# Performance work log

Hardware: AMD Instinct MI355X
Metric: run time of the kernel (lower is better)

Reference implementation:

```python
import jax, jax.numpy as jnp
import numpy as np

STRIDE = 1
PAD = 1
K = 3
BN_EPS = 1e-5


def conv2d(x, w, b, stride, padding):
    out = jax.lax.conv_general_dilated(
        x, w, (stride, stride), [(padding, padding), (padding, padding)],
        dimension_numbers=("NCHW", "OIHW", "NCHW"))
    return out + b[None, :, None, None]


def _bilinear_gather(xb, sy, sx):
    # Zero-fill outside bounds (torchvision DeformConv2d semantics).
    Hin, Win = xb.shape[1], xb.shape[2]
    y0 = jnp.floor(sy)
    x0 = jnp.floor(sx)
    y1 = y0 + 1.0
    x1 = x0 + 1.0
    wy1 = sy - y0
    wy0 = 1.0 - wy1
    wx1 = sx - x0
    wx0 = 1.0 - wx1

    def g(yi, xi):
        valid = (yi >= 0) & (yi < Hin) & (xi >= 0) & (xi < Win)
        yc = jnp.clip(yi, 0, Hin - 1).astype(jnp.int32)
        xc = jnp.clip(xi, 0, Win - 1).astype(jnp.int32)
        v = xb[:, yc, xc]  # [C, K2, Hout, Wout]
        return v * valid[None].astype(xb.dtype)

    return (g(y0, x0) * (wy0 * wx0)[None] + g(y0, x1) * (wy0 * wx1)[None]
            + g(y1, x0) * (wy1 * wx0)[None] + g(y1, x1) * (wy1 * wx1)[None])


def deform_conv2d(x, offset, w, b, stride, padding):
    B, C, Hin, Win = x.shape
    O = w.shape[0]
    K2 = K * K
    Hout, Wout = offset.shape[2], offset.shape[3]
    # torchvision layout: channel 2*k = dy, 2*k+1 = dx, k row-major over kernel
    off = offset.reshape(B, K2, 2, Hout, Wout)
    dy, dx = off[:, :, 0], off[:, :, 1]
    ki, kj = jnp.meshgrid(jnp.arange(K), jnp.arange(K), indexing="ij")
    ki = ki.reshape(K2).astype(x.dtype)
    kj = kj.reshape(K2).astype(x.dtype)
    oy = (jnp.arange(Hout) * stride - padding).astype(x.dtype)
    ox = (jnp.arange(Wout) * stride - padding).astype(x.dtype)
    sy = ki[None, :, None, None] + oy[None, None, :, None] + dy  # [B,K2,Hout,Wout]
    sx = kj[None, :, None, None] + ox[None, None, None, :] + dx
    sampled = jax.vmap(_bilinear_gather)(x, sy, sx)  # [B, C, K2, Hout, Wout]
    out = jnp.einsum("bckhw,ock->bohw", sampled, w.reshape(O, C, K2))
    return out + b[None, :, None, None]


def batchnorm_train(x, gamma, beta):
    # training-mode BN: biased batch stats over (N, H, W)
    mean = jnp.mean(x, axis=(0, 2, 3), keepdims=True)
    var = jnp.mean(jnp.square(x - mean), axis=(0, 2, 3), keepdims=True)
    xn = (x - mean) * jax.lax.rsqrt(var + BN_EPS)
    return xn * gamma[None, :, None, None] + beta[None, :, None, None]


def setup_inputs() -> dict:
    key = jax.random.key(0)
    ks = jax.random.split(key, 4)
    B, C, H, W = 8, 64, 128, 128
    O = 64
    x = jax.random.normal(ks[0], (B, C, H, W), dtype=jnp.float32)
    fan_off = C * K * K
    offset_w = jax.random.normal(ks[1], (2 * K * K, C, K, K), dtype=jnp.float32) / np.sqrt(fan_off)
    offset_b = jnp.zeros((2 * K * K,), dtype=jnp.float32)
    deform_w = jax.random.normal(ks[2], (O, C, K, K), dtype=jnp.float32) / np.sqrt(fan_off)
    deform_b = jnp.zeros((O,), dtype=jnp.float32)
    bn_gamma = jnp.ones((O,), dtype=jnp.float32)
    bn_beta = jnp.zeros((O,), dtype=jnp.float32)
    prelu_a = jnp.full((1,), 0.2, dtype=jnp.float32)
    return {"x": x, "offset_w": offset_w, "offset_b": offset_b,
            "deform_w": deform_w, "deform_b": deform_b,
            "bn_gamma": bn_gamma, "bn_beta": bn_beta, "prelu_a": prelu_a}


def reference(x, offset_w, offset_b, deform_w, deform_b, bn_gamma, bn_beta, prelu_a):
    offset = conv2d(x, offset_w, offset_b, STRIDE, PAD)
    y = deform_conv2d(x, offset, deform_w, deform_b, STRIDE, PAD)
    y = batchnorm_train(y, bn_gamma, bn_beta)
    return jnp.where(y >= 0, y, prelu_a[0] * y)
```

## Files before the change

### kernel.cpp

```cpp
#include <hip/hip_runtime.h>
#include <hip/hip_bf16.h>
#include <hip/hip_fp16.h>

typedef float f32x4 __attribute__((ext_vector_type(4)));
typedef unsigned int u32;
typedef u32 u32x4 __attribute__((ext_vector_type(4)));
typedef __bf16 bf16x8 __attribute__((ext_vector_type(8)));
typedef short s16x8 __attribute__((ext_vector_type(8)));
typedef unsigned short u16;

#define HWSZ 16384
#define NPIX 131072

#define XT_OFF    0u
#define PART_OFF  33554432u
#define WB_OFF    42991616u
#define STATS_OFF 43106816u
#define WO_OFF    43107840u

__device__ inline u32 pkbf(float lo, float hi) {
  u16 l = __builtin_bit_cast(u16, __float2bfloat16(lo));
  u16 h = __builtin_bit_cast(u16, __float2bfloat16(hi));
  return (u32)l | ((u32)h << 16);
}
__device__ inline float bflo(u32 u) { return __builtin_bit_cast(float, u << 16); }
__device__ inline float bfhi(u32 u) { return __builtin_bit_cast(float, u & 0xFFFF0000u); }

__global__ void kprep(const float* __restrict__ dw, const float* __restrict__ ow,
                      u16* __restrict__ Wb, u16* __restrict__ Wo) {
  int t = blockIdx.x * 256 + threadIdx.x;
  if (t < 36864) {
    int o = t / 576, r = t % 576;
    int c = r / 9, k2 = r % 9;
    __hip_bfloat16 h = __float2bfloat16(dw[t]);
    Wb[o * 576 + k2 * 64 + c] = __builtin_bit_cast(u16, h);
  } else if (t < 55296) {
    int t2 = t - 36864;
    int oc = t2 / 576, r = t2 % 576;
    int c = r / 9, k2 = r % 9;
    float v = (oc < 18) ? ow[(oc * 64 + c) * 9 + k2] : 0.f;
    __hip_bfloat16 h = __float2bfloat16(v);
    Wo[oc * 576 + k2 * 64 + c] = __builtin_bit_cast(u16, h);
  }
}

__global__ void ktrans(const float* __restrict__ x, u16* __restrict__ xt) {
  __shared__ float tile[64][65];
  int blk = blockIdx.x;
  int b = blk >> 8, hwT = (blk & 255) * 64;
  int tid = threadIdx.x;
  int tx = tid & 63, ty = tid >> 6;
  const float* xp = x + (size_t)b * 64 * HWSZ;
#pragma unroll
  for (int r = 0; r < 16; ++r) {
    int c = r * 4 + ty;
    tile[c][tx] = xp[c * HWSZ + hwT + tx];
  }
  __syncthreads();
  u16* xo = xt + ((size_t)b * HWSZ + hwT) * 64;
  int o8 = (tid & 7) * 8;
#pragma unroll
  for (int r = 0; r < 2; ++r) {
    int hwl = r * 32 + (tid >> 3);
    u32x4 out;
#pragma unroll
    for (int j = 0; j < 4; ++j)
      out[j] = pkbf(tile[o8 + 2 * j][hwl], tile[o8 + 2 * j + 1][hwl]);
    *(u32x4*)&xo[(size_t)hwl * 64 + o8] = out;
  }
}

__global__ __launch_bounds__(256, 6) void kmain(
    const u16* __restrict__ xt, const u16* __restrict__ Wo,
    const float* __restrict__ offb, const u16* __restrict__ Wb,
    const float* __restrict__ db, float* __restrict__ y,
    float* __restrict__ part) {
  __shared__ u16 S2[2][64 * 64];
  __shared__ float OFFT[64 * 20];
  __shared__ u32 mWp[576 * 2];
  __shared__ u32 mPos[576];
  int tid = threadIdx.x;
  int lane = tid & 63, wid = tid >> 6;
  int bid = blockIdx.x;
  int batch = bid & 7, tilei = bid >> 3;
  int base = (batch << 14) + tilei * 64;
  int b = batch;
  int hw0 = base & 16383;
  int h0 = hw0 >> 7, w0 = hw0 & 127;

  int oct = lane & 7;
  int p0 = wid * 8 + (lane >> 3);
  int oct16 = oct << 4, oct8 = oct << 3;
  int q8 = (lane >> 4) * 8;
  const char* xb = (const char*)xt;

  int ocb2 = wid & 1, pxb2 = (wid >> 1) * 2;
  int orow_o = ocb2 * 16 + (lane & 15);
  f32x4 acco0 = {0.f, 0.f, 0.f, 0.f}, acco1 = {0.f, 0.f, 0.f, 0.f};
#pragma unroll
  for (int k = 0; k < 9; ++k) {
#pragma unroll
    for (int pi = 0; pi < 2; ++pi) {
      int pp = p0 + pi * 32;
      int yy = h0 - 1 + k / 3, xx = w0 + pp - 1 + k % 3;
      bool v = ((unsigned)yy < 128u) && ((unsigned)xx < 128u);
      const char* pb =
          v ? xb + (size_t)(((b << 14) + yy * 128 + xx) * 128) + oct16 : xb;
      u32x4 g = *(const u32x4*)pb;
      u32 msk = v ? 0xFFFFFFFFu : 0u;
      u32x4 out;
#pragma unroll
      for (int j = 0; j < 4; ++j) out[j] = g[j] & msk;
      *(u32x4*)&S2[k & 1][(pp * 64 + oct8) ^ ((pp & 7) << 3)] = out;
    }
    __syncthreads();
#pragma unroll
    for (int h = 0; h < 2; ++h) {
      int kc = 2 * k + h;
      s16x8 a = *(const s16x8*)(Wo + orow_o * 576 + kc * 32 + q8);
      {
        int row = pxb2 * 16 + (lane & 15);
        int idx = (row * 64 + h * 32 + q8) ^ ((row & 7) << 3);
        bf16x8 bb = __builtin_bit_cast(bf16x8, *(const s16x8*)&S2[k & 1][idx]);
        acco0 = __builtin_amdgcn_mfma_f32_16x16x32_bf16(
            __builtin_bit_cast(bf16x8, a), bb, acco0, 0, 0, 0);
      }
      {
        int row = (pxb2 + 1) * 16 + (lane & 15);
        int idx = (row * 64 + h * 32 + q8) ^ ((row & 7) << 3);
        bf16x8 bb = __builtin_bit_cast(bf16x8, *(const s16x8*)&S2[k & 1][idx]);
        acco1 = __builtin_amdgcn_mfma_f32_16x16x32_bf16(
            __builtin_bit_cast(bf16x8, a), bb, acco1, 0, 0, 0);
      }
    }
  }
  __syncthreads();

#pragma unroll
  for (int t2 = 0; t2 < 2; ++t2) {
    int pixl = (pxb2 + t2) * 16 + (lane & 15);
    int ocb = ocb2 * 16 + (lane >> 4) * 4;
    f32x4 a = t2 ? acco1 : acco0;
#pragma unroll
    for (int r = 0; r < 4; ++r) {
      int oc = ocb + r;
      if (oc < 18) OFFT[pixl * 20 + oc] = a[r] + offb[oc];
    }
  }
  __syncthreads();

  for (int t = tid; t < 576; t += 256) {
    int tp = t / 9, k2 = t - tp * 9;
    int pix = base + tp;
    int hw = pix & 16383;
    int hh = hw >> 7, ww = hw & 127;
    float dy = OFFT[tp * 20 + 2 * k2];
    float dx = OFFT[tp * 20 + 2 * k2 + 1];
    float sy = (float)(hh - 1 + k2 / 3) + dy;
    float sx = (float)(ww - 1 + k2 % 3) + dx;
    float fy = floorf(sy), fx = floorf(sx);
    int y0 = (int)fy, x0 = (int)fx;
    float wy1 = sy - fy, wx1 = sx - fx;
    float ay0 = ((unsigned)y0 < 128u) ? 1.f - wy1 : 0.f;
    float ay1 = ((unsigned)(y0 + 1) < 128u) ? wy1 : 0.f;
    float ax0 = ((unsigned)x0 < 128u) ? 1.f - wx1 : 0.f;
    float ax1 = ((unsigned)(x0 + 1) < 128u) ? wx1 : 0.f;
    int y0c = min(max(y0, 0), 127), x0c = min(max(x0, 0), 127);
    int dys = min(max(y0 + 1, 0), 127) - y0c;
    int dxs = min(max(x0 + 1, 0), 127) - x0c;
    mWp[t * 2]     = __builtin_bit_cast(u32, __floats2half2_rn(ay0 * ax0, ay0 * ax1));
    mWp[t * 2 + 1] = __builtin_bit_cast(u32, __floats2half2_rn(ay1 * ax0, ay1 * ax1));
    mPos[t] = (u32)(((b << 14) + y0c * 128 + x0c) * 128) | (u32)dxs | ((u32)dys << 1);
  }
  __syncthreads();

  f32x4 acc[4];
#pragma unroll
  for (int nb = 0; nb < 4; ++nb) acc[nb] = {0.f, 0.f, 0.f, 0.f};
  int orow_d = wid * 16 + (lane & 15);
#pragma unroll
  for (int k = 0; k < 9; ++k) {
#pragma unroll
    for (int pi = 0; pi < 2; ++pi) {
      int pp = p0 + pi * 32;
      int t = pp * 9 + k;
      u32 wlo = mWp[t * 2], whi = mWp[t * 2 + 1];
      u32 pm = mPos[t];
      u32 dxB = (pm & 1u) << 7;
      u32 dyB = (pm & 2u) << 13;
      const char* pb = xb + (pm & 0xFFFFFF80u) + oct16;
      u32x4 c00 = *(const u32x4*)pb;
      u32x4 c01 = *(const u32x4*)(pb + dxB);
      u32x4 c10 = *(const u32x4*)(pb + dyB);
      u32x4 c11 = *(const u32x4*)(pb + dyB + dxB);
      __half2 hl = __builtin_bit_cast(__half2, wlo);
      __half2 hh2 = __builtin_bit_cast(__half2, whi);
      float w00 = __low2float(hl), w01 = __high2float(hl);
      float w10 = __low2float(hh2), w11 = __high2float(hh2);
      u32x4 out;
#pragma unroll
      for (int j = 0; j < 4; ++j) {
        float sL = fmaf(w11, bflo(c11[j]), fmaf(w10, bflo(c10[j]),
                   fmaf(w01, bflo(c01[j]), w00 * bflo(c00[j]))));
        float sH = fmaf(w11, bfhi(c11[j]), fmaf(w10, bfhi(c10[j]),
                   fmaf(w01, bfhi(c01[j]), w00 * bfhi(c00[j]))));
        out[j] = pkbf(sL, sH);
      }
      *(u32x4*)&S2[k & 1][(pp * 64 + oct8) ^ ((pp & 7) << 3)] = out;
    }
    __syncthreads();
#pragma unroll
    for (int h = 0; h < 2; ++h) {
      int kc = 2 * k + h;
      s16x8 a = *(const s16x8*)(Wb + orow_d * 576 + kc * 32 + q8);
#pragma unroll
      for (int nb = 0; nb < 4; ++nb) {
        int row = nb * 16 + (lane & 15);
        int idx = (row * 64 + h * 32 + q8) ^ ((row & 7) << 3);
        bf16x8 bb = __builtin_bit_cast(bf16x8, *(const s16x8*)&S2[k & 1][idx]);
        acc[nb] = __builtin_amdgcn_mfma_f32_16x16x32_bf16(
            __builtin_bit_cast(bf16x8, a), bb, acc[nb], 0, 0, 0);
      }
    }
  }

  int obase = wid * 16 + (lane >> 4) * 4;
  float s1[4] = {0, 0, 0, 0}, s2[4] = {0, 0, 0, 0};
#pragma unroll
  for (int nb = 0; nb < 4; ++nb) {
    int pix = base + nb * 16 + (lane & 15);
    int hw = pix & 16383;
    float* yp = y + (size_t)b * (64 * HWSZ) + hw;
#pragma unroll
    for (int r = 0; r < 4; ++r) {
      int o = obase + r;
      float v = acc[nb][r] + db[o];
      yp[(size_t)o * HWSZ] = v;
      s1[r] += v;
      s2[r] += v * v;
    }
  }
#pragma unroll
  for (int m = 1; m < 16; m <<= 1) {
#pragma unroll
    for (int r = 0; r < 4; ++r) {
      s1[r] += __shfl_xor(s1[r], m, 64);
      s2[r] += __shfl_xor(s2[r], m, 64);
    }
  }
  if ((lane & 15) == 0) {
    float* pp = part + (size_t)bid * 128;
#pragma unroll
    for (int r = 0; r < 4; ++r) {
      pp[obase + r] = s1[r];
      pp[64 + obase + r] = s2[r];
    }
  }
}

__global__ void kbnf(const float* __restrict__ part, const float* __restrict__ gamma,
                     const float* __restrict__ beta, float* __restrict__ stats) {
  __shared__ float r1[256], r2[256];
  int o = blockIdx.x;
  int tid = threadIdx.x;
  float s1 = 0.f, s2 = 0.f;
  for (int i = tid; i < 2048; i += 256) {
    s1 += part[(size_t)i * 128 + o];
    s2 += part[(size_t)i * 128 + 64 + o];
  }
  r1[tid] = s1; r2[tid] = s2;
  __syncthreads();
  for (int s = 128; s > 0; s >>= 1) {
    if (tid < s) { r1[tid] += r1[tid + s]; r2[tid] += r2[tid + s]; }
    __syncthreads();
  }
  if (tid == 0) {
    float m = r1[0] * (1.f / 131072.f);
    float v = r2[0] * (1.f / 131072.f) - m * m;
    float sc = gamma[o] * rsqrtf(v + 1e-5f);
    stats[128 + o] = sc;
    stats[192 + o] = beta[o] - m * sc;
  }
}

__global__ void kfinal(float* __restrict__ y, const float* __restrict__ stats,
                       const float* __restrict__ pa) {
  float a = pa[0];
  int total = NPIX * 64 / 4;
  for (int i = blockIdx.x * blockDim.x + threadIdx.x; i < total;
       i += gridDim.x * blockDim.x) {
    int o = (i >> 12) & 63;
    f32x4 v = ((const f32x4*)y)[i];
    float sc = stats[128 + o], sh = stats[192 + o];
#pragma unroll
    for (int j = 0; j < 4; ++j) {
      float t = fmaf(v[j], sc, sh);
      v[j] = t >= 0.f ? t : a * t;
    }
    ((f32x4*)y)[i] = v;
  }
}

extern "C" void kernel_launch(void* const* d_in, const int* in_sizes, int n_in,
                              void* d_out, int out_size, void* d_ws, size_t ws_size,
                              hipStream_t stream) {
  const float* x  = (const float*)d_in[0];
  const float* ow = (const float*)d_in[1];
  const float* ob = (const float*)d_in[2];
  const float* dw = (const float*)d_in[3];
  const float* db = (const float*)d_in[4];
  const float* gm = (const float*)d_in[5];
  const float* bt = (const float*)d_in[6];
  const float* pa = (const float*)d_in[7];
  char* ws = (char*)d_ws;
  u16*   xt    = (u16*)(ws + XT_OFF);
  float* part  = (float*)(ws + PART_OFF);
  u16*   Wb    = (u16*)(ws + WB_OFF);
  u16*   Wo    = (u16*)(ws + WO_OFF);
  float* stats = (float*)(ws + STATS_OFF);
  float* y = (float*)d_out;

  kprep<<<216, 256, 0, stream>>>(dw, ow, Wb, Wo);
  ktrans<<<2048, 256, 0, stream>>>(x, xt);
  kmain<<<2048, 256, 0, stream>>>(xt, Wo, ob, Wb, db, y, part);
  kbnf<<<64, 256, 0, stream>>>(part, gm, bt, stats);
  kfinal<<<2048, 256, 0, stream>>>(y, stats, pa);
}
```

Baseline: 98.11 us.

## Prefetch next tap's global gathers into registers and relax occupancy bound

Both the offset-conv im2col loop and the deformable bilinear-gather loop are software-pipelined. The global loads for tap k+1 are issued into a second register set before tap k is blended and stored to shared memory, so memory latency overlaps the MFMA work. To make room for the extra live registers, the launch-bounds occupancy hint drops from 6 to 4 blocks. The OFFT offset table is aliased onto the S2 staging buffer to cut shared memory. The risk is that fewer resident waves hide latency worse than the explicit prefetch recovers it.

Measured after the change: 97.92 us. No clear change (-0.2%).

```diff
diff --git a/kernel.cpp b/kernel.cpp
--- a/kernel.cpp
+++ b/kernel.cpp
@@ -70,15 +70,15 @@
   }
 }
 
-__global__ __launch_bounds__(256, 6) void kmain(
+__global__ __launch_bounds__(256, 4) void kmain(
     const u16* __restrict__ xt, const u16* __restrict__ Wo,
     const float* __restrict__ offb, const u16* __restrict__ Wb,
     const float* __restrict__ db, float* __restrict__ y,
     float* __restrict__ part) {
   __shared__ u16 S2[2][64 * 64];
-  __shared__ float OFFT[64 * 20];
   __shared__ u32 mWp[576 * 2];
   __shared__ u32 mPos[576];
+  float* OFFT = (float*)&S2[0][0];
   int tid = threadIdx.x;
   int lane = tid & 63, wid = tid >> 6;
   int bid = blockIdx.x;
@@ -97,8 +97,8 @@
   int ocb2 = wid & 1, pxb2 = (wid >> 1) * 2;
   int orow_o = ocb2 * 16 + (lane & 15);
   f32x4 acco0 = {0.f, 0.f, 0.f, 0.f}, acco1 = {0.f, 0.f, 0.f, 0.f};
-#pragma unroll
-  for (int k = 0; k < 9; ++k) {
+
+  auto im_load = [&](int k, u32x4 (&g)[2], u32 (&m)[2]) {
 #pragma unroll
     for (int pi = 0; pi < 2; ++pi) {
       int pp = p0 + pi * 32;
@@ -106,31 +106,53 @@
       bool v = ((unsigned)yy < 128u) && ((unsigned)xx < 128u);
       const char* pb =
           v ? xb + (size_t)(((b << 14) + yy * 128 + xx) * 128) + oct16 : xb;
-      u32x4 g = *(const u32x4*)pb;
-      u32 msk = v ? 0xFFFFFFFFu : 0u;
+      g[pi] = *(const u32x4*)pb;
+      m[pi] = v ? 0xFFFFFFFFu : 0u;
+    }
+  };
+  auto im_store = [&](int k, const u32x4 (&g)[2], const u32 (&m)[2]) {
+#pragma unroll
+    for (int pi = 0; pi < 2; ++pi) {
+      int pp = p0 + pi * 32;
       u32x4 out;
 #pragma unroll
-      for (int j = 0; j < 4; ++j) out[j] = g[j] & msk;
+      for (int j = 0; j < 4; ++j) out[j] = g[pi][j] & m[pi];
       *(u32x4*)&S2[k & 1][(pp * 64 + oct8) ^ ((pp & 7) << 3)] = out;
     }
-    __syncthreads();
-#pragma unroll
-    for (int h = 0; h < 2; ++h) {
-      int kc = 2 * k + h;
-      s16x8 a = *(const s16x8*)(Wo + orow_o * 576 + kc * 32 + q8);
-      {
-        int row = pxb2 * 16 + (lane & 15);
-        int idx = (row * 64 + h * 32 + q8) ^ ((row & 7) << 3);
-        bf16x8 bb = __builtin_bit_cast(bf16x8, *(const s16x8*)&S2[k & 1][idx]);
-        acco0 = __builtin_amdgcn_mfma_f32_16x16x32_bf16(
-            __builtin_bit_cast(bf16x8, a), bb, acco0, 0, 0, 0);
-      }
-      {
-        int row = (pxb2 + 1) * 16 + (lane & 15);
-        int idx = (row * 64 + h * 32 + q8) ^ ((row & 7) << 3);
-        bf16x8 bb = __builtin_bit_cast(bf16x8, *(const s16x8*)&S2[k & 1][idx]);
-        acco1 = __builtin_amdgcn_mfma_f32_16x16x32_bf16(
-            __builtin_bit_cast(bf16x8, a), bb, acco1, 0, 0, 0);
+  };
+
+  {
+    u32x4 gA[2], gB[2];
+    u32 mA[2], mB[2];
+    im_load(0, gA, mA);
+#pragma unroll
+    for (int k = 0; k < 9; ++k) {
+      if (k & 1) {
+        if (k < 8) im_load(k + 1, gA, mA);
+        im_store(k, gB, mB);
+      } else {
+        if (k < 8) im_load(k + 1, gB, mB);
+        im_store(k, gA, mA);
+      }
+      __syncthreads();
+#pragma unroll
+      for (int h = 0; h < 2; ++h) {
+        int kc = 2 * k + h;
+        s16x8 a = *(const s16x8*)(Wo + orow_o * 576 + kc * 32 + q8);
+        {
+          int row = pxb2 * 16 + (lane & 15);
+          int idx = (row * 64 + h * 32 + q8) ^ ((row & 7) << 3);
+          bf16x8 bb = __builtin_bit_cast(bf16x8, *(const s16x8*)&S2[k & 1][idx]);
+          acco0 = __builtin_amdgcn_mfma_f32_16x16x32_bf16(
+              __builtin_bit_cast(bf16x8, a), bb, acco0, 0, 0, 0);
+        }
+        {
+          int row = (pxb2 + 1) * 16 + (lane & 15);
+          int idx = (row * 64 + h * 32 + q8) ^ ((row & 7) << 3);
+          bf16x8 bb = __builtin_bit_cast(bf16x8, *(const s16x8*)&S2[k & 1][idx]);
+          acco1 = __builtin_amdgcn_mfma_f32_16x16x32_bf16(
+              __builtin_bit_cast(bf16x8, a), bb, acco1, 0, 0, 0);
+        }
       }
     }
   }
@@ -178,48 +200,72 @@
 #pragma unroll
   for (int nb = 0; nb < 4; ++nb) acc[nb] = {0.f, 0.f, 0.f, 0.f};
   int orow_d = wid * 16 + (lane & 15);
-#pragma unroll
-  for (int k = 0; k < 9; ++k) {
+
+  auto tap_load = [&](int k, u32x4 (&c)[2][4], u32 (&wl)[2], u32 (&wh)[2]) {
 #pragma unroll
     for (int pi = 0; pi < 2; ++pi) {
       int pp = p0 + pi * 32;
       int t = pp * 9 + k;
-      u32 wlo = mWp[t * 2], whi = mWp[t * 2 + 1];
+      wl[pi] = mWp[t * 2];
+      wh[pi] = mWp[t * 2 + 1];
       u32 pm = mPos[t];
       u32 dxB = (pm & 1u) << 7;
       u32 dyB = (pm & 2u) << 13;
       const char* pb = xb + (pm & 0xFFFFFF80u) + oct16;
-      u32x4 c00 = *(const u32x4*)pb;
-      u32x4 c01 = *(const u32x4*)(pb + dxB);
-      u32x4 c10 = *(const u32x4*)(pb + dyB);
-      u32x4 c11 = *(const u32x4*)(pb + dyB + dxB);
-      __half2 hl = __builtin_bit_cast(__half2, wlo);
-      __half2 hh2 = __builtin_bit_cast(__half2, whi);
+      c[pi][0] = *(const u32x4*)pb;
+      c[pi][1] = *(const u32x4*)(pb + dxB);
+      c[pi][2] = *(const u32x4*)(pb + dyB);
+      c[pi][3] = *(const u32x4*)(pb + dyB + dxB);
+    }
+  };
+  auto tap_store = [&](int k, const u32x4 (&c)[2][4], const u32 (&wl)[2],
+                       const u32 (&wh)[2]) {
+#pragma unroll
+    for (int pi = 0; pi < 2; ++pi) {
+      int pp = p0 + pi * 32;
+      __half2 hl = __builtin_bit_cast(__half2, wl[pi]);
+      __half2 hh2 = __builtin_bit_cast(__half2, wh[pi]);
       float w00 = __low2float(hl), w01 = __high2float(hl);
       float w10 = __low2float(hh2), w11 = __high2float(hh2);
       u32x4 out;
 #pragma unroll
       for (int j = 0; j < 4; ++j) {
-        float sL = fmaf(w11, bflo(c11[j]), fmaf(w10, bflo(c10[j]),
-                   fmaf(w01, bflo(c01[j]), w00 * bflo(c00[j]))));
-        float sH = fmaf(w11, bfhi(c11[j]), fmaf(w10, bfhi(c10[j]),
-                   fmaf(w01, bfhi(c01[j]), w00 * bfhi(c00[j]))));
+        float sL = fmaf(w11, bflo(c[pi][3][j]), fmaf(w10, bflo(c[pi][2][j]),
+                   fmaf(w01, bflo(c[pi][1][j]), w00 * bflo(c[pi][0][j]))));
+        float sH = fmaf(w11, bfhi(c[pi][3][j]), fmaf(w10, bfhi(c[pi][2][j]),
+                   fmaf(w01, bfhi(c[pi][1][j]), w00 * bfhi(c[pi][0][j]))));
         out[j] = pkbf(sL, sH);
       }
       *(u32x4*)&S2[k & 1][(pp * 64 + oct8) ^ ((pp & 7) << 3)] = out;
     }
-    __syncthreads();
-#pragma unroll
-    for (int h = 0; h < 2; ++h) {
-      int kc = 2 * k + h;
-      s16x8 a = *(const s16x8*)(Wb + orow_d * 576 + kc * 32 + q8);
-#pragma unroll
-      for (int nb = 0; nb < 4; ++nb) {
-        int row = nb * 16 + (lane & 15);
-        int idx = (row * 64 + h * 32 + q8) ^ ((row & 7) << 3);
-        bf16x8 bb = __builtin_bit_cast(bf16x8, *(const s16x8*)&S2[k & 1][idx]);
-        acc[nb] = __builtin_amdgcn_mfma_f32_16x16x32_bf16(
-            __builtin_bit_cast(bf16x8, a), bb, acc[nb], 0, 0, 0);
+  };
+
+  {
+    u32x4 cA[2][4], cB[2][4];
+    u32 wlA[2], whA[2], wlB[2], whB[2];
+    tap_load(0, cA, wlA, whA);
+#pragma unroll
+    for (int k = 0; k < 9; ++k) {
+      if (k & 1) {
+        if (k < 8) tap_load(k + 1, cA, wlA, whA);
+        tap_store(k, cB, wlB, whB);
+      } else {
+        if (k < 8) tap_load(k + 1, cB, wlB, whB);
+        tap_store(k, cA, wlA, whA);
+      }
+      __syncthreads();
+#pragma unroll
+      for (int h = 0; h < 2; ++h) {
+        int kc = 2 * k + h;
+        s16x8 a = *(const s16x8*)(Wb + orow_d * 576 + kc * 32 + q8);
+#pragma unroll
+        for (int nb = 0; nb < 4; ++nb) {
+          int row = nb * 16 + (lane & 15);
+          int idx = (row * 64 + h * 32 + q8) ^ ((row & 7) << 3);
+          bf16x8 bb = __builtin_bit_cast(bf16x8, *(const s16x8*)&S2[k & 1][idx]);
+          acc[nb] = __builtin_amdgcn_mfma_f32_16x16x32_bf16(
+              __builtin_bit_cast(bf16x8, a), bb, acc[nb], 0, 0, 0);
+        }
       }
     }
   }
```

## Give each wave its own 16-pixel slice to remove block-wide barriers

Applied to the files above, without the earlier changes.

Reworks the fused offset-conv and deformable-conv kernel so each wave gathers, interpolates and multiplies its own 16 pixels against all output channels, using a per-wave LDS slice. This drops every __syncthreads in the main loops, since each wave only reads LDS data it wrote itself. In exchange, each wave now loads all weight rows from global memory, the launch-bounds occupancy hint drops from 6 to 4, and the BN partial-stats buffer grows fourfold (per wave instead of per block), so the finalize kernel reads more partials.

After: 172.5 us. 1.76x slower.

```diff
diff --git a/kernel.cpp b/kernel.cpp
--- a/kernel.cpp
+++ b/kernel.cpp
@@ -70,12 +70,12 @@
   }
 }
 
-__global__ __launch_bounds__(256, 6) void kmain(
+__global__ __launch_bounds__(256, 4) void kmain(
     const u16* __restrict__ xt, const u16* __restrict__ Wo,
     const float* __restrict__ offb, const u16* __restrict__ Wb,
     const float* __restrict__ db, float* __restrict__ y,
     float* __restrict__ part) {
-  __shared__ u16 S2[2][64 * 64];
+  __shared__ u16 S2[2][4 * 1024];
   __shared__ float OFFT[64 * 20];
   __shared__ u32 mWp[576 * 2];
   __shared__ u32 mPos[576];
@@ -88,74 +88,69 @@
   int hw0 = base & 16383;
   int h0 = hw0 >> 7, w0 = hw0 & 127;
 
-  int oct = lane & 7;
-  int p0 = wid * 8 + (lane >> 3);
-  int oct16 = oct << 4, oct8 = oct << 3;
+  int pl = lane >> 2;
+  int quad = lane & 3;
+  int qb = quad << 5;
+  int q16 = quad << 4;
+  int sw = (pl & 7) << 3;
+  int pxg = w0 + wid * 16 + pl;
   int q8 = (lane >> 4) * 8;
   const char* xb = (const char*)xt;
 
-  int ocb2 = wid & 1, pxb2 = (wid >> 1) * 2;
-  int orow_o = ocb2 * 16 + (lane & 15);
-  f32x4 acco0 = {0.f, 0.f, 0.f, 0.f}, acco1 = {0.f, 0.f, 0.f, 0.f};
+  f32x4 acco[2];
+  acco[0] = {0.f, 0.f, 0.f, 0.f};
+  acco[1] = {0.f, 0.f, 0.f, 0.f};
 #pragma unroll
   for (int k = 0; k < 9; ++k) {
-#pragma unroll
-    for (int pi = 0; pi < 2; ++pi) {
-      int pp = p0 + pi * 32;
-      int yy = h0 - 1 + k / 3, xx = w0 + pp - 1 + k % 3;
+    u16* Sw = &S2[k & 1][wid * 1024];
+    {
+      int yy = h0 - 1 + k / 3, xx = pxg - 1 + k % 3;
       bool v = ((unsigned)yy < 128u) && ((unsigned)xx < 128u);
       const char* pb =
-          v ? xb + (size_t)(((b << 14) + yy * 128 + xx) * 128) + oct16 : xb;
-      u32x4 g = *(const u32x4*)pb;
+          v ? xb + (size_t)(((b << 14) + yy * 128 + xx) * 128) + qb : xb;
+      u32x4 g0 = *(const u32x4*)pb;
+      u32x4 g1 = *(const u32x4*)(pb + 16);
       u32 msk = v ? 0xFFFFFFFFu : 0u;
-      u32x4 out;
-#pragma unroll
-      for (int j = 0; j < 4; ++j) out[j] = g[j] & msk;
-      *(u32x4*)&S2[k & 1][(pp * 64 + oct8) ^ ((pp & 7) << 3)] = out;
-    }
-    __syncthreads();
+      u32x4 o0, o1;
+#pragma unroll
+      for (int j = 0; j < 4; ++j) { o0[j] = g0[j] & msk; o1[j] = g1[j] & msk; }
+      *(u32x4*)&Sw[(pl * 64 + q16) ^ sw] = o0;
+      *(u32x4*)&Sw[(pl * 64 + q16 + 8) ^ sw] = o1;
+    }
 #pragma unroll
     for (int h = 0; h < 2; ++h) {
       int kc = 2 * k + h;
-      s16x8 a = *(const s16x8*)(Wo + orow_o * 576 + kc * 32 + q8);
-      {
-        int row = pxb2 * 16 + (lane & 15);
-        int idx = (row * 64 + h * 32 + q8) ^ ((row & 7) << 3);
-        bf16x8 bb = __builtin_bit_cast(bf16x8, *(const s16x8*)&S2[k & 1][idx]);
-        acco0 = __builtin_amdgcn_mfma_f32_16x16x32_bf16(
-            __builtin_bit_cast(bf16x8, a), bb, acco0, 0, 0, 0);
-      }
-      {
-        int row = (pxb2 + 1) * 16 + (lane & 15);
-        int idx = (row * 64 + h * 32 + q8) ^ ((row & 7) << 3);
-        bf16x8 bb = __builtin_bit_cast(bf16x8, *(const s16x8*)&S2[k & 1][idx]);
-        acco1 = __builtin_amdgcn_mfma_f32_16x16x32_bf16(
-            __builtin_bit_cast(bf16x8, a), bb, acco1, 0, 0, 0);
-      }
-    }
-  }
-  __syncthreads();
-
-#pragma unroll
-  for (int t2 = 0; t2 < 2; ++t2) {
-    int pixl = (pxb2 + t2) * 16 + (lane & 15);
-    int ocb = ocb2 * 16 + (lane >> 4) * 4;
-    f32x4 a = t2 ? acco1 : acco0;
+#pragma unroll
+      for (int ob = 0; ob < 2; ++ob) {
+        s16x8 a = *(const s16x8*)(Wo + (ob * 16 + (lane & 15)) * 576 + kc * 32 + q8);
+        int row = lane & 15;
+        bf16x8 bb = __builtin_bit_cast(
+            bf16x8, *(const s16x8*)&Sw[(row * 64 + h * 32 + q8) ^ ((row & 7) << 3)]);
+        acco[ob] = __builtin_amdgcn_mfma_f32_16x16x32_bf16(
+            __builtin_bit_cast(bf16x8, a), bb, acco[ob], 0, 0, 0);
+      }
+    }
+  }
+
+#pragma unroll
+  for (int ob = 0; ob < 2; ++ob) {
+    int pixl = wid * 16 + (lane & 15);
+    int ocb = ob * 16 + (lane >> 4) * 4;
 #pragma unroll
     for (int r = 0; r < 4; ++r) {
       int oc = ocb + r;
-      if (oc < 18) OFFT[pixl * 20 + oc] = a[r] + offb[oc];
-    }
-  }
-  __syncthreads();
-
-  for (int t = tid; t < 576; t += 256) {
+      if (oc < 18) OFFT[pixl * 20 + oc] = acco[ob][r] + offb[oc];
+    }
+  }
+
+  for (int t = lane; t < 144; t += 64) {
     int tp = t / 9, k2 = t - tp * 9;
-    int pix = base + tp;
+    int pixl = wid * 16 + tp;
+    int pix = base + pixl;
     int hw = pix & 16383;
     int hh = hw >> 7, ww = hw & 127;
-    float dy = OFFT[tp * 20 + 2 * k2];
-    float dx = OFFT[tp * 20 + 2 * k2 + 1];
+    float dy = OFFT[pixl * 20 + 2 * k2];
+    float dx = OFFT[pixl * 20 + 2 * k2 + 1];
     float sy = (float)(hh - 1 + k2 / 3) + dy;
     float sx = (float)(ww - 1 + k2 % 3) + dx;
     float fy = floorf(sy), fx = floorf(sx);
@@ -168,92 +163,105 @@
     int y0c = min(max(y0, 0), 127), x0c = min(max(x0, 0), 127);
     int dys = min(max(y0 + 1, 0), 127) - y0c;
     int dxs = min(max(x0 + 1, 0), 127) - x0c;
-    mWp[t * 2]     = __builtin_bit_cast(u32, __floats2half2_rn(ay0 * ax0, ay0 * ax1));
-    mWp[t * 2 + 1] = __builtin_bit_cast(u32, __floats2half2_rn(ay1 * ax0, ay1 * ax1));
-    mPos[t] = (u32)(((b << 14) + y0c * 128 + x0c) * 128) | (u32)dxs | ((u32)dys << 1);
-  }
-  __syncthreads();
+    int tg = pixl * 9 + k2;
+    mWp[tg * 2]     = __builtin_bit_cast(u32, __floats2half2_rn(ay0 * ax0, ay0 * ax1));
+    mWp[tg * 2 + 1] = __builtin_bit_cast(u32, __floats2half2_rn(ay1 * ax0, ay1 * ax1));
+    mPos[tg] = (u32)(((b << 14) + y0c * 128 + x0c) * 128) | (u32)dxs | ((u32)dys << 1);
+  }
 
   f32x4 acc[4];
 #pragma unroll
-  for (int nb = 0; nb < 4; ++nb) acc[nb] = {0.f, 0.f, 0.f, 0.f};
-  int orow_d = wid * 16 + (lane & 15);
+  for (int ob = 0; ob < 4; ++ob) acc[ob] = {0.f, 0.f, 0.f, 0.f};
 #pragma unroll
   for (int k = 0; k < 9; ++k) {
-#pragma unroll
-    for (int pi = 0; pi < 2; ++pi) {
-      int pp = p0 + pi * 32;
-      int t = pp * 9 + k;
-      u32 wlo = mWp[t * 2], whi = mWp[t * 2 + 1];
-      u32 pm = mPos[t];
+    u16* Sw = &S2[k & 1][wid * 1024];
+    {
+      int tg = (wid * 16 + pl) * 9 + k;
+      u32 wlo = mWp[tg * 2], whi = mWp[tg * 2 + 1];
+      u32 pm = mPos[tg];
       u32 dxB = (pm & 1u) << 7;
       u32 dyB = (pm & 2u) << 13;
-      const char* pb = xb + (pm & 0xFFFFFF80u) + oct16;
-      u32x4 c00 = *(const u32x4*)pb;
-      u32x4 c01 = *(const u32x4*)(pb + dxB);
-      u32x4 c10 = *(const u32x4*)(pb + dyB);
-      u32x4 c11 = *(const u32x4*)(pb + dyB + dxB);
+      const char* pb = xb + (pm & 0xFFFFFF80u) + qb;
+      u32x4 a00 = *(const u32x4*)pb;
+      u32x4 b00 = *(const u32x4*)(pb + 16);
+      u32x4 a01 = *(const u32x4*)(pb + dxB);
+      u32x4 b01 = *(const u32x4*)(pb + dxB + 16);
+      u32x4 a10 = *(const u32x4*)(pb + dyB);
+      u32x4 b10 = *(const u32x4*)(pb + dyB + 16);
+      u32x4 a11 = *(const u32x4*)(pb + dyB + dxB);
+      u32x4 b11 = *(const u32x4*)(pb + dyB + dxB + 16);
       __half2 hl = __builtin_bit_cast(__half2, wlo);
       __half2 hh2 = __builtin_bit_cast(__half2, whi);
       float w00 = __low2float(hl), w01 = __high2float(hl);
       float w10 = __low2float(hh2), w11 = __high2float(hh2);
-      u32x4 out;
+      u32x4 o0, o1;
 #pragma unroll
       for (int j = 0; j < 4; ++j) {
-        float sL = fmaf(w11, bflo(c11[j]), fmaf(w10, bflo(c10[j]),
-                   fmaf(w01, bflo(c01[j]), w00 * bflo(c00[j]))));
-        float sH = fmaf(w11, bfhi(c11[j]), fmaf(w10, bfhi(c10[j]),
-                   fmaf(w01, bfhi(c01[j]), w00 * bfhi(c00[j]))));
-        out[j] = pkbf(sL, sH);
-      }
-      *(u32x4*)&S2[k & 1][(pp * 64 + oct8) ^ ((pp & 7) << 3)] = out;
-    }
-    __syncthreads();
+        float sL = fmaf(w11, bflo(a11[j]), fmaf(w10, bflo(a10[j]),
+                   fmaf(w01, bflo(a01[j]), w00 * bflo(a00[j]))));
+        float sH = fmaf(w11, bfhi(a11[j]), fmaf(w10, bfhi(a10[j]),
+                   fmaf(w01, bfhi(a01[j]), w00 * bfhi(a00[j]))));
+        o0[j] = pkbf(sL, sH);
+        float tL = fmaf(w11, bflo(b11[j]), fmaf(w10, bflo(b10[j]),
+                   fmaf(w01, bflo(b01[j]), w00 * bflo(b00[j]))));
+        float tH = fmaf(w11, bfhi(b11[j]), fmaf(w10, bfhi(b10[j]),
+                   fmaf(w01, bfhi(b01[j]), w00 * bfhi(b00[j]))));
+        o1[j] = pkbf(tL, tH);
+      }
+      *(u32x4*)&Sw[(pl * 64 + q16) ^ sw] = o0;
+      *(u32x4*)&Sw[(pl * 64 + q16 + 8) ^ sw] = o1;
+    }
 #pragma unroll
     for (int h = 0; h < 2; ++h) {
       int kc = 2 * k + h;
-      s16x8 a = *(const s16x8*)(Wb + orow_d * 576 + kc * 32 + q8);
-#pragma unroll
-      for (int nb = 0; nb < 4; ++nb) {
-        int row = nb * 16 + (lane & 15);
-        int idx = (row * 64 + h * 32 + q8) ^ ((row & 7) << 3);
-        bf16x8 bb = __builtin_bit_cast(bf16x8, *(const s16x8*)&S2[k & 1][idx]);
-        acc[nb] = __builtin_amdgcn_mfma_f32_16x16x32_bf16(
-            __builtin_bit_cast(bf16x8, a), bb, acc[nb], 0, 0, 0);
-      }
-    }
-  }
-
-  int obase = wid * 16 + (lane >> 4) * 4;
-  float s1[4] = {0, 0, 0, 0}, s2[4] = {0, 0, 0, 0};
-#pragma unroll
-  for (int nb = 0; nb < 4; ++nb) {
-    int pix = base + nb * 16 + (lane & 15);
-    int hw = pix & 16383;
-    float* yp = y + (size_t)b * (64 * HWSZ) + hw;
+#pragma unroll
+      for (int ob = 0; ob < 4; ++ob) {
+        s16x8 a = *(const s16x8*)(Wb + (ob * 16 + (lane & 15)) * 576 + kc * 32 + q8);
+        int row = lane & 15;
+        bf16x8 bb = __builtin_bit_cast(
+            bf16x8, *(const s16x8*)&Sw[(row * 64 + h * 32 + q8) ^ ((row & 7) << 3)]);
+        acc[ob] = __builtin_amdgcn_mfma_f32_16x16x32_bf16(
+            __builtin_bit_cast(bf16x8, a), bb, acc[ob], 0, 0, 0);
+      }
+    }
+  }
+
+  int pix = base + wid * 16 + (lane & 15);
+  int hw = pix & 16383;
+  float* yp = y + (size_t)b * (64 * HWSZ) + hw;
+  float s1[4][4], s2[4][4];
+#pragma unroll
+  for (int ob = 0; ob < 4; ++ob) {
+    int ocb = ob * 16 + (lane >> 4) * 4;
 #pragma unroll
     for (int r = 0; r < 4; ++r) {
-      int o = obase + r;
-      float v = acc[nb][r] + db[o];
+      int o = ocb + r;
+      float v = acc[ob][r] + db[o];
       yp[(size_t)o * HWSZ] = v;
-      s1[r] += v;
-      s2[r] += v * v;
+      s1[ob][r] = v;
+      s2[ob][r] = v * v;
     }
   }
 #pragma unroll
   for (int m = 1; m < 16; m <<= 1) {
 #pragma unroll
-    for (int r = 0; r < 4; ++r) {
-      s1[r] += __shfl_xor(s1[r], m, 64);
-      s2[r] += __shfl_xor(s2[r], m, 64);
-    }
+    for (int ob = 0; ob < 4; ++ob)
+#pragma unroll
+      for (int r = 0; r < 4; ++r) {
+        s1[ob][r] += __shfl_xor(s1[ob][r], m, 64);
+        s2[ob][r] += __shfl_xor(s2[ob][r], m, 64);
+      }
   }
   if ((lane & 15) == 0) {
-    float* pp = part + (size_t)bid * 128;
-#pragma unroll
-    for (int r = 0; r < 4; ++r) {
-      pp[obase + r] = s1[r];
-      pp[64 + obase + r] = s2[r];
+    float* pp = part + (size_t)bid * 512 + wid * 128;
+#pragma unroll
+    for (int ob = 0; ob < 4; ++ob) {
+      int ocb = ob * 16 + (lane >> 4) * 4;
+#pragma unroll
+      for (int r = 0; r < 4; ++r) {
+        pp[ocb + r] = s1[ob][r];
+        pp[64 + ocb + r] = s2[ob][r];
+      }
     }
   }
 }
@@ -264,7 +272,7 @@
   int o = blockIdx.x;
   int tid = threadIdx.x;
   float s1 = 0.f, s2 = 0.f;
-  for (int i = tid; i < 2048; i += 256) {
+  for (int i = tid; i < 8192; i += 256) {
     s1 += part[(size_t)i * 128 + o];
     s2 += part[(size_t)i * 128 + 64 + o];
   }
```

## Use full-row 128-pixel tiles and stage pre-BN output in bf16

Applied to the files above, without the earlier changes.

Each kmain block now processes a whole 128-pixel image row instead of 64 pixels, which halves the grid and doubles the MFMA work per block, letting one A-fragment load feed more MFMAs. OFFT now aliases the S2 buffer to save shared memory, and occupancy is lowered to 4 blocks. The pre-BN activations are written to a bf16 workspace instead of fp32 output, and the final BN+PReLU pass reads bf16 and expands to fp32, cutting intermediate memory traffic. The cost is extra rounding of pre-normalization values and higher register and LDS pressure per block.

Result: faster. 92.27 us, median of 2 (-5.9%).

```diff
diff --git a/kernel.cpp b/kernel.cpp
--- a/kernel.cpp
+++ b/kernel.cpp
@@ -13,6 +13,7 @@
 #define NPIX 131072
 
 #define XT_OFF    0u
+#define YB_OFF    16777216u
 #define PART_OFF  33554432u
 #define WB_OFF    42991616u
 #define STATS_OFF 43106816u
@@ -70,23 +71,22 @@
   }
 }
 
-__global__ __launch_bounds__(256, 6) void kmain(
+__global__ __launch_bounds__(256, 4) void kmain(
     const u16* __restrict__ xt, const u16* __restrict__ Wo,
     const float* __restrict__ offb, const u16* __restrict__ Wb,
-    const float* __restrict__ db, float* __restrict__ y,
+    const float* __restrict__ db, u16* __restrict__ yb,
     float* __restrict__ part) {
-  __shared__ u16 S2[2][64 * 64];
-  __shared__ float OFFT[64 * 20];
-  __shared__ u32 mWp[576 * 2];
-  __shared__ u32 mPos[576];
+  __shared__ u16 S2[2][128 * 64];
+  __shared__ u32 mWp[1152 * 2];
+  __shared__ u32 mPos[1152];
+  float* OFFT = (float*)&S2[0][0];
   int tid = threadIdx.x;
   int lane = tid & 63, wid = tid >> 6;
   int bid = blockIdx.x;
   int batch = bid & 7, tilei = bid >> 3;
-  int base = (batch << 14) + tilei * 64;
+  int base = (batch << 14) + tilei * 128;
   int b = batch;
-  int hw0 = base & 16383;
-  int h0 = hw0 >> 7, w0 = hw0 & 127;
+  int h0 = tilei;
 
   int oct = lane & 7;
   int p0 = wid * 8 + (lane >> 3);
@@ -94,15 +94,17 @@
   int q8 = (lane >> 4) * 8;
   const char* xb = (const char*)xt;
 
-  int ocb2 = wid & 1, pxb2 = (wid >> 1) * 2;
+  int ocb2 = wid & 1, pxb4 = (wid >> 1) * 4;
   int orow_o = ocb2 * 16 + (lane & 15);
-  f32x4 acco0 = {0.f, 0.f, 0.f, 0.f}, acco1 = {0.f, 0.f, 0.f, 0.f};
+  f32x4 acco[4];
+#pragma unroll
+  for (int t2 = 0; t2 < 4; ++t2) acco[t2] = {0.f, 0.f, 0.f, 0.f};
 #pragma unroll
   for (int k = 0; k < 9; ++k) {
 #pragma unroll
-    for (int pi = 0; pi < 2; ++pi) {
+    for (int pi = 0; pi < 4; ++pi) {
       int pp = p0 + pi * 32;
-      int yy = h0 - 1 + k / 3, xx = w0 + pp - 1 + k % 3;
+      int yy = h0 - 1 + k / 3, xx = pp - 1 + k % 3;
       bool v = ((unsigned)yy < 128u) && ((unsigned)xx < 128u);
       const char* pb =
           v ? xb + (size_t)(((b << 14) + yy * 128 + xx) * 128) + oct16 : xb;
@@ -118,38 +120,31 @@
     for (int h = 0; h < 2; ++h) {
       int kc = 2 * k + h;
       s16x8 a = *(const s16x8*)(Wo + orow_o * 576 + kc * 32 + q8);
-      {
-        int row = pxb2 * 16 + (lane & 15);
+#pragma unroll
+      for (int t2 = 0; t2 < 4; ++t2) {
+        int row = (pxb4 + t2) * 16 + (lane & 15);
         int idx = (row * 64 + h * 32 + q8) ^ ((row & 7) << 3);
         bf16x8 bb = __builtin_bit_cast(bf16x8, *(const s16x8*)&S2[k & 1][idx]);
-        acco0 = __builtin_amdgcn_mfma_f32_16x16x32_bf16(
-            __builtin_bit_cast(bf16x8, a), bb, acco0, 0, 0, 0);
+        acco[t2] = __builtin_amdgcn_mfma_f32_16x16x32_bf16(
+            __builtin_bit_cast(bf16x8, a), bb, acco[t2], 0, 0, 0);
       }
-      {
-        int row = (pxb2 + 1) * 16 + (lane & 15);
-        int idx = (row * 64 + h * 32 + q8) ^ ((row & 7) << 3);
-        bf16x8 bb = __builtin_bit_cast(bf16x8, *(const s16x8*)&S2[k & 1][idx]);
-        acco1 = __builtin_amdgcn_mfma_f32_16x16x32_bf16(
-            __builtin_bit_cast(bf16x8, a), bb, acco1, 0, 0, 0);
-      }
-    }
-  }
-  __syncthreads();
-
-#pragma unroll
-  for (int t2 = 0; t2 < 2; ++t2) {
-    int pixl = (pxb2 + t2) * 16 + (lane & 15);
+    }
+  }
+  __syncthreads();
+
+#pragma unroll
+  for (int t2 = 0; t2 < 4; ++t2) {
+    int pixl = (pxb4 + t2) * 16 + (lane & 15);
     int ocb = ocb2 * 16 + (lane >> 4) * 4;
-    f32x4 a = t2 ? acco1 : acco0;
 #pragma unroll
     for (int r = 0; r < 4; ++r) {
       int oc = ocb + r;
-      if (oc < 18) OFFT[pixl * 20 + oc] = a[r] + offb[oc];
-    }
-  }
-  __syncthreads();
-
-  for (int t = tid; t < 576; t += 256) {
+      if (oc < 18) OFFT[pixl * 20 + oc] = acco[t2][r] + offb[oc];
+    }
+  }
+  __syncthreads();
+
+  for (int t = tid; t < 1152; t += 256) {
     int tp = t / 9, k2 = t - tp * 9;
     int pix = base + tp;
     int hw = pix & 16383;
@@ -174,14 +169,14 @@
   }
   __syncthreads();
 
-  f32x4 acc[4];
-#pragma unroll
-  for (int nb = 0; nb < 4; ++nb) acc[nb] = {0.f, 0.f, 0.f, 0.f};
+  f32x4 acc[8];
+#pragma unroll
+  for (int nb = 0; nb < 8; ++nb) acc[nb] = {0.f, 0.f, 0.f, 0.f};
   int orow_d = wid * 16 + (lane & 15);
 #pragma unroll
   for (int k = 0; k < 9; ++k) {
 #pragma unroll
-    for (int pi = 0; pi < 2; ++pi) {
+    for (int pi = 0; pi < 4; ++pi) {
       int pp = p0 + pi * 32;
       int t = pp * 9 + k;
       u32 wlo = mWp[t * 2], whi = mWp[t * 2 + 1];
@@ -214,7 +209,7 @@
       int kc = 2 * k + h;
       s16x8 a = *(const s16x8*)(Wb + orow_d * 576 + kc * 32 + q8);
 #pragma unroll
-      for (int nb = 0; nb < 4; ++nb) {
+      for (int nb = 0; nb < 8; ++nb) {
         int row = nb * 16 + (lane & 15);
         int idx = (row * 64 + h * 32 + q8) ^ ((row & 7) << 3);
         bf16x8 bb = __builtin_bit_cast(bf16x8, *(const s16x8*)&S2[k & 1][idx]);
@@ -227,15 +222,15 @@
   int obase = wid * 16 + (lane >> 4) * 4;
   float s1[4] = {0, 0, 0, 0}, s2[4] = {0, 0, 0, 0};
 #pragma unroll
-  for (int nb = 0; nb < 4; ++nb) {
+  for (int nb = 0; nb < 8; ++nb) {
     int pix = base + nb * 16 + (lane & 15);
     int hw = pix & 16383;
-    float* yp = y + (size_t)b * (64 * HWSZ) + hw;
+    u16* yp = yb + (size_t)b * (64 * HWSZ) + hw;
 #pragma unroll
     for (int r = 0; r < 4; ++r) {
       int o = obase + r;
       float v = acc[nb][r] + db[o];
-      yp[(size_t)o * HWSZ] = v;
+      yp[(size_t)o * HWSZ] = __builtin_bit_cast(u16, __float2bfloat16(v));
       s1[r] += v;
       s2[r] += v * v;
     }
@@ -264,7 +259,7 @@
   int o = blockIdx.x;
   int tid = threadIdx.x;
   float s1 = 0.f, s2 = 0.f;
-  for (int i = tid; i < 2048; i += 256) {
+  for (int i = tid; i < 1024; i += 256) {
     s1 += part[(size_t)i * 128 + o];
     s2 += part[(size_t)i * 128 + 64 + o];
   }
@@ -283,21 +278,27 @@
   }
 }
 
-__global__ void kfinal(float* __restrict__ y, const float* __restrict__ stats,
-                       const float* __restrict__ pa) {
+__global__ void kfinal(const u16* __restrict__ yb, float* __restrict__ y,
+                       const float* __restrict__ stats, const float* __restrict__ pa) {
   float a = pa[0];
-  int total = NPIX * 64 / 4;
+  int total = NPIX * 64 / 8;
   for (int i = blockIdx.x * blockDim.x + threadIdx.x; i < total;
        i += gridDim.x * blockDim.x) {
-    int o = (i >> 12) & 63;
-    f32x4 v = ((const f32x4*)y)[i];
+    int o = (i >> 11) & 63;
+    u32x4 v = ((const u32x4*)yb)[i];
     float sc = stats[128 + o], sh = stats[192 + o];
+    f32x4 o0, o1;
 #pragma unroll
     for (int j = 0; j < 4; ++j) {
-      float t = fmaf(v[j], sc, sh);
-      v[j] = t >= 0.f ? t : a * t;
-    }
-    ((f32x4*)y)[i] = v;
+      float tL = fmaf(bflo(v[j]), sc, sh);
+      float tH = fmaf(bfhi(v[j]), sc, sh);
+      float rL = tL >= 0.f ? tL : a * tL;
+      float rH = tH >= 0.f ? tH : a * tH;
+      if (j < 2) { o0[2 * j] = rL; o0[2 * j + 1] = rH; }
+      else       { o1[2 * (j - 2)] = rL; o1[2 * (j - 2) + 1] = rH; }
+    }
+    ((f32x4*)y)[2 * i] = o0;
+    ((f32x4*)y)[2 * i + 1] = o1;
   }
 }
 
@@ -314,6 +315,7 @@
   const float* pa = (const float*)d_in[7];
   char* ws = (char*)d_ws;
   u16*   xt    = (u16*)(ws + XT_OFF);
+  u16*   yb    = (u16*)(ws + YB_OFF);
   float* part  = (float*)(ws + PART_OFF);
   u16*   Wb    = (u16*)(ws + WB_OFF);
   u16*   Wo    = (u16*)(ws + WO_OFF);
@@ -322,7 +324,7 @@
 
   kprep<<<216, 256, 0, stream>>>(dw, ow, Wb, Wo);
   ktrans<<<2048, 256, 0, stream>>>(x, xt);
-  kmain<<<2048, 256, 0, stream>>>(xt, Wo, ob, Wb, db, y, part);
+  kmain<<<1024, 256, 0, stream>>>(xt, Wo, ob, Wb, db, yb, part);
   kbnf<<<64, 256, 0, stream>>>(part, gm, bt, stats);
-  kfinal<<<2048, 256, 0, stream>>>(y, stats, pa);
-}
+  kfinal<<<2048, 256, 0, stream>>>(yb, y, stats, pa);
+}
```
